# Kernel tuning notes

Hardware: AMD Instinct MI355X
Metric: run time of the kernel (lower is better)

## Reference

```python
import jax, jax.numpy as jnp
import numpy as np

EPS = 1e-5

def conv1x1(x, w, b):
    # x: [B,C,H,W], w: [O,C], b: [O]
    return jnp.einsum('bchw,oc->bohw', x, w) + b[None, :, None, None]

def bn_eval(x, w, b, m, v):
    inv = w / jnp.sqrt(v + EPS)
    return (x - m[None, :, None, None]) * inv[None, :, None, None] + b[None, :, None, None]

def setup_inputs() -> dict:
    key = jax.random.key(0)
    ks = jax.random.split(key, 32)
    B, Fg, Fl, Fi, H, W = 4, 128, 128, 64, 64, 64
    d = {}
    d['g'] = jax.random.normal(ks[0], (B, Fg, H, W), jnp.float32)
    d['x'] = jax.random.normal(ks[1], (B, Fl, H, W), jnp.float32)
    d['wg_w'] = jax.random.normal(ks[2], (Fi, Fg), jnp.float32) * 0.1
    d['wg_b'] = jax.random.normal(ks[3], (Fi,), jnp.float32) * 0.1
    d['bng_w'] = jax.random.uniform(ks[4], (Fi,), jnp.float32)
    d['bng_b'] = jax.random.normal(ks[5], (Fi,), jnp.float32) * 0.1
    d['bng_m'] = jax.random.normal(ks[6], (Fi,), jnp.float32) * 0.1
    d['bng_v'] = jax.random.uniform(ks[7], (Fi,), jnp.float32) + 0.5
    d['wx_w'] = jax.random.normal(ks[8], (Fi, Fl), jnp.float32) * 0.1
    d['wx_b'] = jax.random.normal(ks[9], (Fi,), jnp.float32) * 0.1
    d['bnx_w'] = jax.random.uniform(ks[10], (Fi,), jnp.float32)
    d['bnx_b'] = jax.random.normal(ks[11], (Fi,), jnp.float32) * 0.1
    d['bnx_m'] = jax.random.normal(ks[12], (Fi,), jnp.float32) * 0.1
    d['bnx_v'] = jax.random.uniform(ks[13], (Fi,), jnp.float32) + 0.5
    d['q_w'] = jax.random.normal(ks[14], (Fi // 8, Fi), jnp.float32) * 0.1
    d['q_b'] = jax.random.normal(ks[15], (Fi // 8,), jnp.float32) * 0.1
    d['k_w'] = jax.random.normal(ks[16], (Fi // 8, Fi), jnp.float32) * 0.1
    d['k_b'] = jax.random.normal(ks[17], (Fi // 8,), jnp.float32) * 0.1
    d['v_w'] = jax.random.normal(ks[18], (Fi, Fi), jnp.float32) * 0.1
    d['v_b'] = jax.random.normal(ks[19], (Fi,), jnp.float32) * 0.1
    d['sa_gamma'] = jax.random.normal(ks[20], (1,), jnp.float32)
    d['psi_w'] = jax.random.normal(ks[21], (1, Fi), jnp.float32) * 0.1
    d['psi_b'] = jax.random.normal(ks[22], (1,), jnp.float32) * 0.1
    d['bnp_w'] = jax.random.uniform(ks[23], (1,), jnp.float32)
    d['bnp_b'] = jax.random.normal(ks[24], (1,), jnp.float32) * 0.1
    d['bnp_m'] = jax.random.normal(ks[25], (1,), jnp.float32) * 0.1
    d['bnp_v'] = jax.random.uniform(ks[26], (1,), jnp.float32) + 0.5
    return d

def reference(g, x, wg_w, wg_b, bng_w, bng_b, bng_m, bng_v,
              wx_w, wx_b, bnx_w, bnx_b, bnx_m, bnx_v,
              q_w, q_b, k_w, k_b, v_w, v_b, sa_gamma,
              psi_w, psi_b, bnp_w, bnp_b, bnp_m, bnp_v):
    g1 = bn_eval(conv1x1(g, wg_w, wg_b), bng_w, bng_b, bng_m, bng_v)
    x1 = bn_eval(conv1x1(x, wx_w, wx_b), bnx_w, bnx_b, bnx_m, bnx_v)
    c = jax.nn.relu(g1 + x1)  # [B, Fi, H, W]
    B, C, H, W = c.shape
    N = H * W
    q = conv1x1(c, q_w, q_b).reshape(B, -1, N)  # [B, Fi/8, N]
    k = conv1x1(c, k_w, k_b).reshape(B, -1, N)
    v = conv1x1(c, v_w, v_b).reshape(B, C, N)
    energy = jnp.einsum('bcn,bcm->bnm', q, k)    # [B, N, N]
    attn = jax.nn.softmax(energy, axis=-1)
    sa_out = jnp.einsum('bcm,bnm->bcn', v, attn).reshape(B, C, H, W)
    attended = sa_gamma[0] * sa_out + c
    psi = jax.nn.sigmoid(bn_eval(conv1x1(attended, psi_w, psi_b), bnp_w, bnp_b, bnp_m, bnp_v))
    return x * psi
```

## Files before the change

kernel.cpp:

```cpp
#include <hip/hip_runtime.h>
#include <hip/hip_bf16.h>


typedef short bf16x8 __attribute__((ext_vector_type(8)));
typedef unsigned short u16x8 __attribute__((ext_vector_type(8)));
typedef unsigned short u16x4 __attribute__((ext_vector_type(4)));
typedef float f32x4 __attribute__((ext_vector_type(4)));

__device__ __forceinline__ unsigned short f2b(float f) {
  unsigned u = __builtin_bit_cast(unsigned, f);
  u = (u + 0x7FFFu + ((u >> 16) & 1u)) >> 16;
  return (unsigned short)u;
}

#define EPSV 1e-5f

#define WCAT_OFF   0u
#define WQKV_OFF   32768u
#define BIASC_OFF  44032u
#define BIASQ_OFF  44288u
#define PSIW_OFF   44608u
#define SCAL_OFF   44864u
#define C_OFF      45056u
#define Q_OFF      (C_OFF + 4194304u)
#define K_OFF      (Q_OFF + 262144u)
#define V_OFF      (K_OFF + 262144u)
#define OPART_OFF  (V_OFF + 2097152u)
#define ML_OFF     (OPART_OFF + 16777216u)

__global__ __launch_bounds__(256) void prep_kernel(
    const float* __restrict__ wg_w, const float* __restrict__ wg_b,
    const float* __restrict__ bng_w, const float* __restrict__ bng_b,
    const float* __restrict__ bng_m, const float* __restrict__ bng_v,
    const float* __restrict__ wx_w, const float* __restrict__ wx_b,
    const float* __restrict__ bnx_w, const float* __restrict__ bnx_b,
    const float* __restrict__ bnx_m, const float* __restrict__ bnx_v,
    const float* __restrict__ q_w, const float* __restrict__ q_b,
    const float* __restrict__ k_w, const float* __restrict__ k_b,
    const float* __restrict__ v_w, const float* __restrict__ v_b,
    const float* __restrict__ psi_w, const float* __restrict__ psi_b,
    const float* __restrict__ bnp_w, const float* __restrict__ bnp_b,
    const float* __restrict__ bnp_m, const float* __restrict__ bnp_v,
    const float* __restrict__ sa_gamma,
    unsigned short* __restrict__ Wcat, unsigned short* __restrict__ Wqkv,
    float* __restrict__ bias_c, float* __restrict__ bias_q,
    float* __restrict__ psi_w2, float* __restrict__ scal)
{
  const int t = threadIdx.x;
  const int bid = blockIdx.x;
  if (bid < 16) {
    int o = bid * 4 + (t >> 6);
    int k = (t & 63) * 4;
    float inv;
    const float* src;
    if (k < 128) {
      inv = bng_w[o] * rsqrtf(bng_v[o] + EPSV);
      src = wg_w + o * 128 + k;
    } else {
      inv = bnx_w[o] * rsqrtf(bnx_v[o] + EPSV);
      src = wx_w + o * 128 + (k - 128);
    }
    float4 wv = *(const float4*)src;
    u16x4 pk;
    pk[0] = f2b(wv.x * inv); pk[1] = f2b(wv.y * inv);
    pk[2] = f2b(wv.z * inv); pk[3] = f2b(wv.w * inv);
    *(u16x4*)(Wcat + o * 256 + k) = pk;
    return;
  }
  for (int idx = t; idx < 80 * 64; idx += 256) {
    int r = idx >> 6, k = idx & 63;
    float wv;
    if (r < 8)       wv = q_w[r * 64 + k];
    else if (r < 16) wv = k_w[(r - 8) * 64 + k];
    else             wv = v_w[(r - 16) * 64 + k];
    Wqkv[idx] = f2b(wv);
  }
  if (t < 64) {
    int o = t;
    float invg = bng_w[o] * rsqrtf(bng_v[o] + EPSV);
    float invx = bnx_w[o] * rsqrtf(bnx_v[o] + EPSV);
    bias_c[o] = (wg_b[o] - bng_m[o]) * invg + bng_b[o]
              + (wx_b[o] - bnx_m[o]) * invx + bnx_b[o];
    float invp = bnp_w[0] * rsqrtf(bnp_v[0] + EPSV);
    psi_w2[o] = psi_w[o] * invp;
  }
  if (t < 80)
    bias_q[t] = (t < 8) ? q_b[t] : (t < 16 ? k_b[t - 8] : v_b[t - 16]);
  if (t == 0) {
    float invp = bnp_w[0] * rsqrtf(bnp_v[0] + EPSV);
    scal[0] = sa_gamma[0];
    scal[1] = (psi_b[0] - bnp_m[0]) * invp + bnp_b[0];
  }
}

__global__ __launch_bounds__(256) void conv_qkv_kernel(
    const float* __restrict__ g, const float* __restrict__ x,
    const unsigned short* __restrict__ Wcat, const unsigned short* __restrict__ Wqkv,
    const float* __restrict__ bias_c, const float* __restrict__ bias_q,
    float* __restrict__ c_out, unsigned short* __restrict__ Qb,
    unsigned short* __restrict__ Kb, unsigned short* __restrict__ Vb)
{
  __shared__ __attribute__((aligned(16))) unsigned short xt[32][264];
  __shared__ __attribute__((aligned(16))) unsigned short clds[32][72];

  const int t = threadIdx.x;
  const int bid = blockIdx.x;
  const int b = bid >> 7;
  const int n0 = (bid & 127) << 5;

  {
    const int col4 = t & 7;
    const int rowg = t >> 3;
    float4 v[8];
    #pragma unroll
    for (int rr = 0; rr < 8; ++rr) {
      int row = rowg * 8 + rr;
      const float* src = (row < 128)
          ? (g + ((size_t)(b * 128 + row)) * 4096 + n0 + col4 * 4)
          : (x + ((size_t)(b * 128 + (row - 128))) * 4096 + n0 + col4 * 4);
      v[rr] = *(const float4*)src;
    }
    #pragma unroll
    for (int j = 0; j < 4; ++j) {
      u16x8 pk;
      #pragma unroll
      for (int rr = 0; rr < 8; ++rr)
        pk[rr] = f2b(((const float*)&v[rr])[j]);
      *(u16x8*)(&xt[col4 * 4 + j][rowg * 8]) = pk;
    }
  }
  __syncthreads();

  const int l = t & 63, w = t >> 6;
  const int l15 = l & 15, lg = l >> 4;
  f32x4 zf = {0.f, 0.f, 0.f, 0.f};

  f32x4 acc[2];
  acc[0] = acc[1] = zf;
  const int orow = w * 16 + l15;
  #pragma unroll
  for (int ks = 0; ks < 8; ++ks) {
    bf16x8 af = *(const bf16x8*)(Wcat + orow * 256 + ks * 32 + lg * 8);
    #pragma unroll
    for (int ns = 0; ns < 2; ++ns) {
      bf16x8 bfv = *(const bf16x8*)(&xt[ns * 16 + l15][ks * 32 + lg * 8]);
      acc[ns] = __builtin_amdgcn_mfma_f32_16x16x32_bf16(af, bfv, acc[ns], 0, 0, 0);
    }
  }
  #pragma unroll
  for (int r = 0; r < 4; ++r) {
    int o = w * 16 + lg * 4 + r;
    float bc = bias_c[o];
    #pragma unroll
    for (int ns = 0; ns < 2; ++ns) {
      float cv = fmaxf(acc[ns][r] + bc, 0.f);
      int n = ns * 16 + l15;
      c_out[((size_t)(b * 64 + o)) * 4096 + n0 + n] = cv;
      clds[n][o] = f2b(cv);
    }
  }
  __syncthreads();

  #pragma unroll
  for (int i = 0; i < 3; ++i) {
    int tau = w + 4 * i;
    if (tau >= 10) break;
    int t5 = tau % 5, ns = tau / 5;
    f32x4 a2 = zf;
    #pragma unroll
    for (int kk = 0; kk < 2; ++kk) {
      bf16x8 af = *(const bf16x8*)(Wqkv + (t5 * 16 + l15) * 64 + kk * 32 + lg * 8);
      bf16x8 bfv = *(const bf16x8*)(&clds[ns * 16 + l15][kk * 32 + lg * 8]);
      a2 = __builtin_amdgcn_mfma_f32_16x16x32_bf16(af, bfv, a2, 0, 0, 0);
    }
    #pragma unroll
    for (int r = 0; r < 4; ++r) {
      int row = t5 * 16 + lg * 4 + r;
      int ngl = n0 + ns * 16 + l15;
      float val = a2[r] + bias_q[row];
      if (t5 == 0) {
        if (row < 8) Qb[(((size_t)b << 12) + ngl) * 8 + row] = f2b(val);
        else         Kb[(((size_t)b << 12) + ngl) * 8 + (row - 8)] = f2b(val);
      } else {
        int vch = (t5 - 1) * 16 + lg * 4 + r;
        Vb[((size_t)(b * 64 + vch)) * 4096 + ngl] = f2b(val);
      }
    }
  }
}

__global__ __launch_bounds__(256) void attn_partial_kernel(
    const unsigned short* __restrict__ Qb, const unsigned short* __restrict__ Kb,
    const unsigned short* __restrict__ Vb,
    float* __restrict__ Opart, float* __restrict__ ml)
{
  __shared__ __attribute__((aligned(16))) unsigned short klds[64][8];
  __shared__ __attribute__((aligned(16))) unsigned short vlds[64][72];
  __shared__ __attribute__((aligned(16))) unsigned short plds[4][16][72];

  const int t = threadIdx.x;
  const int bid = blockIdx.x;
  const int qt = bid & 63;
  const int b = (bid >> 6) & 3;
  const int ci = bid >> 8;
  const int n0 = qt << 6;
  const int l = t & 63, w = t >> 6;
  const int l15 = l & 15, lg = l >> 4;

  bf16x8 qf = {0, 0, 0, 0, 0, 0, 0, 0};
  if (lg == 0)
    qf = *(const bf16x8*)(Qb + (((size_t)b << 12) + n0 + w * 16 + l15) * 8);

  f32x4 zf = {0.f, 0.f, 0.f, 0.f};
  f32x4 O[4];
  O[0] = O[1] = O[2] = O[3] = zf;
  float m_run[4] = {-INFINITY, -INFINITY, -INFINITY, -INFINITY};
  float l_run[4] = {0.f, 0.f, 0.f, 0.f};

  const int m_lo = ci << 10, m_hi = (ci + 1) << 10;
  for (int m0 = m_lo; m0 < m_hi; m0 += 64) {
    if (t < 64)
      *(int4*)(&klds[t][0]) = *(const int4*)(Kb + (((size_t)b << 12) + m0 + t) * 8);
    #pragma unroll
    for (int i = 0; i < 2; ++i) {
      int ci2 = t + 256 * i;
      int row = ci2 >> 3, off = ci2 & 7;
      *(int4*)(&vlds[row][off * 8]) =
          *(const int4*)(Vb + ((size_t)(b * 64 + row)) * 4096 + m0 + off * 8);
    }
    __syncthreads();

    f32x4 e[4];
    #pragma unroll
    for (int mt = 0; mt < 4; ++mt) {
      bf16x8 kf = *(const bf16x8*)(&klds[mt * 16 + l15][0]);
      e[mt] = __builtin_amdgcn_mfma_f32_16x16x32_bf16(qf, kf, zf, 0, 0, 0);
    }

    #pragma unroll
    for (int r = 0; r < 4; ++r) {
      float vm = fmaxf(fmaxf(e[0][r], e[1][r]), fmaxf(e[2][r], e[3][r]));
      vm = fmaxf(vm, __shfl_xor(vm, 1));
      vm = fmaxf(vm, __shfl_xor(vm, 2));
      vm = fmaxf(vm, __shfl_xor(vm, 4));
      vm = fmaxf(vm, __shfl_xor(vm, 8));
      float nm = fmaxf(m_run[r], vm);
      float sc = __expf(m_run[r] - nm);
      float s = 0.f;
      #pragma unroll
      for (int mt = 0; mt < 4; ++mt) {
        float p = __expf(e[mt][r] - nm);
        e[mt][r] = p;
        s += p;
      }
      s += __shfl_xor(s, 1);
      s += __shfl_xor(s, 2);
      s += __shfl_xor(s, 4);
      s += __shfl_xor(s, 8);
      l_run[r] = l_run[r] * sc + s;
      m_run[r] = nm;
      #pragma unroll
      for (int mt = 0; mt < 4; ++mt)
        plds[w][lg * 4 + r][mt * 16 + l15] = f2b(e[mt][r]);
      #pragma unroll
      for (int ct = 0; ct < 4; ++ct) O[ct][r] *= sc;
    }

    #pragma unroll
    for (int ct = 0; ct < 4; ++ct) {
      #pragma unroll
      for (int kk = 0; kk < 2; ++kk) {
        bf16x8 pa = *(const bf16x8*)(&plds[w][l15][kk * 32 + lg * 8]);
        bf16x8 vb = *(const bf16x8*)(&vlds[ct * 16 + l15][kk * 32 + lg * 8]);
        O[ct] = __builtin_amdgcn_mfma_f32_16x16x32_bf16(pa, vb, O[ct], 0, 0, 0);
      }
    }
    __syncthreads();
  }

  const size_t pb = ((size_t)(ci * 4 + b)) << 12;
  #pragma unroll
  for (int ct = 0; ct < 4; ++ct) {
    int ch = ct * 16 + l15;
    #pragma unroll
    for (int r = 0; r < 4; ++r) {
      int qg = n0 + w * 16 + lg * 4 + r;
      Opart[(pb + qg) * 64 + ch] = O[ct][r];
    }
  }
  if (l15 == 0) {
    #pragma unroll
    for (int r = 0; r < 4; ++r) {
      int qg = n0 + w * 16 + lg * 4 + r;
      float2 mv;
      mv.x = m_run[r]; mv.y = l_run[r];
      *(float2*)(ml + (pb + qg) * 2) = mv;
    }
  }
}

__global__ __launch_bounds__(256) void combine_kernel(
    const float* __restrict__ Opart, const float* __restrict__ ml,
    const float* __restrict__ c_in, const float* __restrict__ xin,
    const float* __restrict__ psi_w2, const float* __restrict__ scal,
    float* __restrict__ out)
{
  __shared__ __attribute__((aligned(16))) float c_lds[64][68];
  __shared__ float psi_lds[64];

  const int t = threadIdx.x;
  const int bid = blockIdx.x;
  const int b = bid >> 6;
  const int n0 = (bid & 63) << 6;

  #pragma unroll
  for (int i = 0; i < 4; ++i) {
    int idx = t + 256 * i;
    int ch = idx >> 4, c4 = idx & 15;
    float4 cv = *(const float4*)(c_in + ((size_t)(b * 64 + ch)) * 4096 + n0 + c4 * 4);
    *(float4*)(&c_lds[ch][c4 * 4]) = cv;
  }
  __syncthreads();

  const int q = t >> 2, cg = t & 3;
  const int qg = n0 + q;

  float m[4], li[4];
  float M = -INFINITY;
  #pragma unroll
  for (int ci = 0; ci < 4; ++ci) {
    float2 v = *(const float2*)(ml + ((((size_t)(ci * 4 + b)) << 12) + qg) * 2);
    m[ci] = v.x; li[ci] = v.y;
    M = fmaxf(M, v.x);
  }
  float L = 0.f, wgt[4];
  #pragma unroll
  for (int ci = 0; ci < 4; ++ci) {
    wgt[ci] = __expf(m[ci] - M);
    L += wgt[ci] * li[ci];
  }
  float4 o4[4];
  o4[0] = o4[1] = o4[2] = o4[3] = make_float4(0.f, 0.f, 0.f, 0.f);
  #pragma unroll
  for (int ci = 0; ci < 4; ++ci) {
    const float* base = Opart + ((((size_t)(ci * 4 + b)) << 12) + qg) * 64 + cg * 16;
    float wv = wgt[ci];
    #pragma unroll
    for (int k = 0; k < 4; ++k) {
      float4 p = *(const float4*)(base + k * 4);
      o4[k].x += wv * p.x; o4[k].y += wv * p.y;
      o4[k].z += wv * p.z; o4[k].w += wv * p.w;
    }
  }
  const float invL = 1.f / L;
  const float gamma = scal[0], psi_c = scal[1];
  float ps = 0.f;
  #pragma unroll
  for (int k = 0; k < 4; ++k) {
    const float* op = (const float*)&o4[k];
    #pragma unroll
    for (int jj = 0; jj < 4; ++jj) {
      int ch = cg * 16 + k * 4 + jj;
      ps += psi_w2[ch] * (gamma * (op[jj] * invL) + c_lds[ch][q]);
    }
  }
  ps += __shfl_xor(ps, 1);
  ps += __shfl_xor(ps, 2);
  if (cg == 0)
    psi_lds[q] = 1.f / (1.f + __expf(-(ps + psi_c)));
  __syncthreads();

  #pragma unroll
  for (int i = 0; i < 8; ++i) {
    int idx = t + 256 * i;
    int f = idx >> 4, c4 = idx & 15;
    size_t off = ((size_t)(b * 128 + f)) * 4096 + n0 + c4 * 4;
    float4 xv = *(const float4*)(xin + off);
    float4 ov;
    ov.x = xv.x * psi_lds[c4 * 4 + 0];
    ov.y = xv.y * psi_lds[c4 * 4 + 1];
    ov.z = xv.z * psi_lds[c4 * 4 + 2];
    ov.w = xv.w * psi_lds[c4 * 4 + 3];
    *(float4*)(out + off) = ov;
  }
}

extern "C" void kernel_launch(void* const* d_in, const int* in_sizes, int n_in,
                              void* d_out, int out_size, void* d_ws, size_t ws_size,
                              hipStream_t stream) {
  (void)in_sizes; (void)n_in; (void)out_size; (void)ws_size;
  const float* g     = (const float*)d_in[0];
  const float* x     = (const float*)d_in[1];
  const float* wg_w  = (const float*)d_in[2];
  const float* wg_b  = (const float*)d_in[3];
  const float* bng_w = (const float*)d_in[4];
  const float* bng_b = (const float*)d_in[5];
  const float* bng_m = (const float*)d_in[6];
  const float* bng_v = (const float*)d_in[7];
  const float* wx_w  = (const float*)d_in[8];
  const float* wx_b  = (const float*)d_in[9];
  const float* bnx_w = (const float*)d_in[10];
  const float* bnx_b = (const float*)d_in[11];
  const float* bnx_m = (const float*)d_in[12];
  const float* bnx_v = (const float*)d_in[13];
  const float* q_w   = (const float*)d_in[14];
  const float* q_b   = (const float*)d_in[15];
  const float* k_w   = (const float*)d_in[16];
  const float* k_b   = (const float*)d_in[17];
  const float* v_w   = (const float*)d_in[18];
  const float* v_b   = (const float*)d_in[19];
  const float* sa_g  = (const float*)d_in[20];
  const float* psi_w = (const float*)d_in[21];
  const float* psi_b = (const float*)d_in[22];
  const float* bnp_w = (const float*)d_in[23];
  const float* bnp_b = (const float*)d_in[24];
  const float* bnp_m = (const float*)d_in[25];
  const float* bnp_v = (const float*)d_in[26];
  float* out = (float*)d_out;

  char* ws = (char*)d_ws;
  unsigned short* Wcat = (unsigned short*)(ws + WCAT_OFF);
  unsigned short* Wqkv = (unsigned short*)(ws + WQKV_OFF);
  float* bias_c = (float*)(ws + BIASC_OFF);
  float* bias_q = (float*)(ws + BIASQ_OFF);
  float* psiw2  = (float*)(ws + PSIW_OFF);
  float* scal   = (float*)(ws + SCAL_OFF);
  float* c_buf  = (float*)(ws + C_OFF);
  unsigned short* Qb = (unsigned short*)(ws + Q_OFF);
  unsigned short* Kb = (unsigned short*)(ws + K_OFF);
  unsigned short* Vb = (unsigned short*)(ws + V_OFF);
  float* Opart = (float*)(ws + OPART_OFF);
  float* mlb   = (float*)(ws + ML_OFF);

  hipLaunchKernelGGL(prep_kernel, dim3(17), dim3(256), 0, stream,
                     wg_w, wg_b, bng_w, bng_b, bng_m, bng_v,
                     wx_w, wx_b, bnx_w, bnx_b, bnx_m, bnx_v,
                     q_w, q_b, k_w, k_b, v_w, v_b,
                     psi_w, psi_b, bnp_w, bnp_b, bnp_m, bnp_v, sa_g,
                     Wcat, Wqkv, bias_c, bias_q, psiw2, scal);

  hipLaunchKernelGGL(conv_qkv_kernel, dim3(512), dim3(256), 0, stream,
                     g, x, Wcat, Wqkv, bias_c, bias_q, c_buf, Qb, Kb, Vb);

  hipLaunchKernelGGL(attn_partial_kernel, dim3(1024), dim3(256), 0, stream,
                     Qb, Kb, Vb, Opart, mlb);

  hipLaunchKernelGGL(combine_kernel, dim3(256), dim3(256), 0, stream,
                     Opart, mlb, c_buf, x, psiw2, scal, out);
}
```

Before: 188.9 us.

## Store c and partial outputs in bf16, halve tiles, double attention KV splits

Intermediate c and the attention partial outputs are now stored as bf16 rather than fp32, which cuts workspace traffic between kernels. The conv tile shrinks from 32 to 16 pixels and the combine tile from 64 to 16 queries, so those kernels launch more blocks. The attention KV range is split into 8 chunks instead of 4, doubling the grid, and V is staged through LDS for coalesced writes. Rounding c and the partials to bf16 adds precision loss, and combine now reads twice as many partial results.

```diff
diff --git a/kernel.cpp b/kernel.cpp
--- a/kernel.cpp
+++ b/kernel.cpp
@@ -11,6 +11,12 @@
   unsigned u = __builtin_bit_cast(unsigned, f);
   u = (u + 0x7FFFu + ((u >> 16) & 1u)) >> 16;
   return (unsigned short)u;
+}
+__device__ __forceinline__ unsigned short f2b16(float f) {
+  return __builtin_bit_cast(unsigned short, __float2bfloat16(f));
+}
+__device__ __forceinline__ float b2f(unsigned short u) {
+  return __bfloat162float(__builtin_bit_cast(__hip_bfloat16, u));
 }
 
 #define EPSV 1e-5f
@@ -22,7 +28,7 @@
 #define PSIW_OFF   44608u
 #define SCAL_OFF   44864u
 #define C_OFF      45056u
-#define Q_OFF      (C_OFF + 4194304u)
+#define Q_OFF      (C_OFF + 2097152u)
 #define K_OFF      (Q_OFF + 262144u)
 #define V_OFF      (K_OFF + 262144u)
 #define OPART_OFF  (V_OFF + 2097152u)
@@ -97,24 +103,25 @@
     const float* __restrict__ g, const float* __restrict__ x,
     const unsigned short* __restrict__ Wcat, const unsigned short* __restrict__ Wqkv,
     const float* __restrict__ bias_c, const float* __restrict__ bias_q,
-    float* __restrict__ c_out, unsigned short* __restrict__ Qb,
+    unsigned short* __restrict__ cb, unsigned short* __restrict__ Qb,
     unsigned short* __restrict__ Kb, unsigned short* __restrict__ Vb)
 {
-  __shared__ __attribute__((aligned(16))) unsigned short xt[32][264];
-  __shared__ __attribute__((aligned(16))) unsigned short clds[32][72];
+  __shared__ __attribute__((aligned(16))) unsigned short xt[16][264];
+  __shared__ __attribute__((aligned(16))) unsigned short clds[16][72];
+  __shared__ __attribute__((aligned(16))) unsigned short vstage[64][20];
 
   const int t = threadIdx.x;
   const int bid = blockIdx.x;
-  const int b = bid >> 7;
-  const int n0 = (bid & 127) << 5;
+  const int b = bid >> 8;
+  const int n0 = (bid & 255) << 4;
 
   {
-    const int col4 = t & 7;
-    const int rowg = t >> 3;
-    float4 v[8];
-    #pragma unroll
-    for (int rr = 0; rr < 8; ++rr) {
-      int row = rowg * 8 + rr;
+    const int col4 = t & 3;
+    const int rowg = t >> 2;
+    float4 v[4];
+    #pragma unroll
+    for (int rr = 0; rr < 4; ++rr) {
+      int row = rowg * 4 + rr;
       const float* src = (row < 128)
           ? (g + ((size_t)(b * 128 + row)) * 4096 + n0 + col4 * 4)
           : (x + ((size_t)(b * 128 + (row - 128))) * 4096 + n0 + col4 * 4);
@@ -122,11 +129,11 @@
     }
     #pragma unroll
     for (int j = 0; j < 4; ++j) {
-      u16x8 pk;
-      #pragma unroll
-      for (int rr = 0; rr < 8; ++rr)
-        pk[rr] = f2b(((const float*)&v[rr])[j]);
-      *(u16x8*)(&xt[col4 * 4 + j][rowg * 8]) = pk;
+      u16x4 pk;
+      #pragma unroll
+      for (int rr = 0; rr < 4; ++rr)
+        pk[rr] = f2b16(((const float*)&v[rr])[j]);
+      *(u16x4*)(&xt[col4 * 4 + j][rowg * 4]) = pk;
     }
   }
   __syncthreads();
@@ -135,64 +142,67 @@
   const int l15 = l & 15, lg = l >> 4;
   f32x4 zf = {0.f, 0.f, 0.f, 0.f};
 
-  f32x4 acc[2];
-  acc[0] = acc[1] = zf;
+  f32x4 acc = zf;
   const int orow = w * 16 + l15;
   #pragma unroll
   for (int ks = 0; ks < 8; ++ks) {
     bf16x8 af = *(const bf16x8*)(Wcat + orow * 256 + ks * 32 + lg * 8);
-    #pragma unroll
-    for (int ns = 0; ns < 2; ++ns) {
-      bf16x8 bfv = *(const bf16x8*)(&xt[ns * 16 + l15][ks * 32 + lg * 8]);
-      acc[ns] = __builtin_amdgcn_mfma_f32_16x16x32_bf16(af, bfv, acc[ns], 0, 0, 0);
-    }
+    bf16x8 bfv = *(const bf16x8*)(&xt[l15][ks * 32 + lg * 8]);
+    acc = __builtin_amdgcn_mfma_f32_16x16x32_bf16(af, bfv, acc, 0, 0, 0);
   }
   #pragma unroll
   for (int r = 0; r < 4; ++r) {
     int o = w * 16 + lg * 4 + r;
-    float bc = bias_c[o];
-    #pragma unroll
-    for (int ns = 0; ns < 2; ++ns) {
-      float cv = fmaxf(acc[ns][r] + bc, 0.f);
-      int n = ns * 16 + l15;
-      c_out[((size_t)(b * 64 + o)) * 4096 + n0 + n] = cv;
-      clds[n][o] = f2b(cv);
-    }
+    float cv = fmaxf(acc[r] + bias_c[o], 0.f);
+    unsigned short cv16 = f2b16(cv);
+    cb[((size_t)(b * 64 + o)) * 4096 + n0 + l15] = cv16;
+    clds[l15][o] = cv16;
   }
   __syncthreads();
 
-  #pragma unroll
-  for (int i = 0; i < 3; ++i) {
-    int tau = w + 4 * i;
-    if (tau >= 10) break;
-    int t5 = tau % 5, ns = tau / 5;
+  const int ngl = n0 + l15;
+  #pragma unroll
+  for (int i = 0; i < 2; ++i) {
+    int t5 = w + 4 * i;
+    if (t5 >= 5) break;
     f32x4 a2 = zf;
     #pragma unroll
     for (int kk = 0; kk < 2; ++kk) {
       bf16x8 af = *(const bf16x8*)(Wqkv + (t5 * 16 + l15) * 64 + kk * 32 + lg * 8);
-      bf16x8 bfv = *(const bf16x8*)(&clds[ns * 16 + l15][kk * 32 + lg * 8]);
+      bf16x8 bfv = *(const bf16x8*)(&clds[l15][kk * 32 + lg * 8]);
       a2 = __builtin_amdgcn_mfma_f32_16x16x32_bf16(af, bfv, a2, 0, 0, 0);
     }
-    #pragma unroll
-    for (int r = 0; r < 4; ++r) {
-      int row = t5 * 16 + lg * 4 + r;
-      int ngl = n0 + ns * 16 + l15;
-      float val = a2[r] + bias_q[row];
-      if (t5 == 0) {
-        if (row < 8) Qb[(((size_t)b << 12) + ngl) * 8 + row] = f2b(val);
-        else         Kb[(((size_t)b << 12) + ngl) * 8 + (row - 8)] = f2b(val);
-      } else {
-        int vch = (t5 - 1) * 16 + lg * 4 + r;
-        Vb[((size_t)(b * 64 + vch)) * 4096 + ngl] = f2b(val);
+    if (t5 == 0) {
+      u16x4 pk;
+      #pragma unroll
+      for (int r = 0; r < 4; ++r)
+        pk[r] = f2b16(a2[r] + bias_q[lg * 4 + r]);
+      if (lg < 2)
+        *(u16x4*)(Qb + (((size_t)b << 12) + ngl) * 8 + lg * 4) = pk;
+      else
+        *(u16x4*)(Kb + (((size_t)b << 12) + ngl) * 8 + (lg - 2) * 4) = pk;
+    } else {
+      #pragma unroll
+      for (int r = 0; r < 4; ++r) {
+        int row = t5 * 16 + lg * 4 + r;
+        int vch = row - 16;
+        vstage[vch][l15] = f2b16(a2[r] + bias_q[row]);
       }
     }
+  }
+  __syncthreads();
+
+  {
+    int row = t >> 2, seg = t & 3;
+    u16x4 pv = *(const u16x4*)(&vstage[row][seg * 4]);
+    *(u16x4*)(Vb + ((size_t)(b * 64 + row)) * 4096 + n0 + seg * 4) = pv;
   }
 }
 
 __global__ __launch_bounds__(256) void attn_partial_kernel(
     const unsigned short* __restrict__ Qb, const unsigned short* __restrict__ Kb,
     const unsigned short* __restrict__ Vb,
-    float* __restrict__ Opart, float* __restrict__ ml)
+    unsigned short* __restrict__ Opart, float* __restrict__ ml)
 {
   __shared__ __attribute__((aligned(16))) unsigned short klds[64][8];
   __shared__ __attribute__((aligned(16))) unsigned short vlds[64][72];
@@ -217,7 +227,7 @@
   float m_run[4] = {-INFINITY, -INFINITY, -INFINITY, -INFINITY};
   float l_run[4] = {0.f, 0.f, 0.f, 0.f};
 
-  const int m_lo = ci << 10, m_hi = (ci + 1) << 10;
+  const int m_lo = ci << 9, m_hi = (ci + 1) << 9;
   for (int m0 = m_lo; m0 < m_hi; m0 += 64) {
     if (t < 64)
       *(int4*)(&klds[t][0]) = *(const int4*)(Kb + (((size_t)b << 12) + m0 + t) * 8);
@@ -261,7 +271,7 @@
       m_run[r] = nm;
       #pragma unroll
       for (int mt = 0; mt < 4; ++mt)
-        plds[w][lg * 4 + r][mt * 16 + l15] = f2b(e[mt][r]);
+        plds[w][lg * 4 + r][mt * 16 + l15] = f2b16(e[mt][r]);
       #pragma unroll
       for (int ct = 0; ct < 4; ++ct) O[ct][r] *= sc;
     }
@@ -285,7 +295,7 @@
     #pragma unroll
     for (int r = 0; r < 4; ++r) {
       int qg = n0 + w * 16 + lg * 4 + r;
-      Opart[(pb + qg) * 64 + ch] = O[ct][r];
+      Opart[(pb + qg) * 64 + ch] = f2b16(O[ct][r]);
     }
   }
   if (l15 == 0) {
@@ -300,80 +310,71 @@
 }
 
 __global__ __launch_bounds__(256) void combine_kernel(
-    const float* __restrict__ Opart, const float* __restrict__ ml,
-    const float* __restrict__ c_in, const float* __restrict__ xin,
+    const unsigned short* __restrict__ Opart, const float* __restrict__ ml,
+    const unsigned short* __restrict__ cb, const float* __restrict__ xin,
     const float* __restrict__ psi_w2, const float* __restrict__ scal,
     float* __restrict__ out)
 {
-  __shared__ __attribute__((aligned(16))) float c_lds[64][68];
-  __shared__ float psi_lds[64];
+  __shared__ __attribute__((aligned(16))) unsigned short c_lds[64][20];
+  __shared__ __attribute__((aligned(8))) float2 ml_lds[16][8];
+  __shared__ float psi_lds[16];
 
   const int t = threadIdx.x;
   const int bid = blockIdx.x;
-  const int b = bid >> 6;
-  const int n0 = (bid & 63) << 6;
-
-  #pragma unroll
-  for (int i = 0; i < 4; ++i) {
-    int idx = t + 256 * i;
-    int ch = idx >> 4, c4 = idx & 15;
-    float4 cv = *(const float4*)(c_in + ((size_t)(b * 64 + ch)) * 4096 + n0 + c4 * 4);
-    *(float4*)(&c_lds[ch][c4 * 4]) = cv;
+  const int b = bid >> 8;
+  const int n0 = (bid & 255) << 4;
+
+  {
+    int row = t >> 2, seg = t & 3;
+    *(u16x4*)(&c_lds[row][seg * 4]) =
+        *(const u16x4*)(cb + ((size_t)(b * 64 + row)) * 4096 + n0 + seg * 4);
+  }
+  if (t < 128) {
+    int q = t >> 3, ci = t & 7;
+    ml_lds[q][ci] = *(const float2*)(ml + ((((size_t)(ci * 4 + b)) << 12) + n0 + q) * 2);
   }
   __syncthreads();
 
-  const int q = t >> 2, cg = t & 3;
+  const int q = t >> 4, cg = t & 15;
   const int qg = n0 + q;
 
-  float m[4], li[4];
   float M = -INFINITY;
   #pragma unroll
-  for (int ci = 0; ci < 4; ++ci) {
-    float2 v = *(const float2*)(ml + ((((size_t)(ci * 4 + b)) << 12) + qg) * 2);
-    m[ci] = v.x; li[ci] = v.y;
-    M = fmaxf(M, v.x);
-  }
-  float L = 0.f, wgt[4];
-  #pragma unroll
-  for (int ci = 0; ci < 4; ++ci) {
-    wgt[ci] = __expf(m[ci] - M);
-    L += wgt[ci] * li[ci];
-  }
-  float4 o4[4];
-  o4[0] = o4[1] = o4[2] = o4[3] = make_float4(0.f, 0.f, 0.f, 0.f);
-  #pragma unroll
-  for (int ci = 0; ci < 4; ++ci) {
-    const float* base = Opart + ((((size_t)(ci * 4 + b)) << 12) + qg) * 64 + cg * 16;
+  for (int ci = 0; ci < 8; ++ci) M = fmaxf(M, ml_lds[q][ci].x);
+  float L = 0.f, wgt[8];
+  #pragma unroll
+  for (int ci = 0; ci < 8; ++ci) {
+    wgt[ci] = __expf(ml_lds[q][ci].x - M);
+    L += wgt[ci] * ml_lds[q][ci].y;
+  }
+  float o4[4] = {0.f, 0.f, 0.f, 0.f};
+  #pragma unroll
+  for (int ci = 0; ci < 8; ++ci) {
+    u16x4 p = *(const u16x4*)(Opart + ((((size_t)(ci * 4 + b)) << 12) + qg) * 64 + cg * 4);
     float wv = wgt[ci];
     #pragma unroll
-    for (int k = 0; k < 4; ++k) {
-      float4 p = *(const float4*)(base + k * 4);
-      o4[k].x += wv * p.x; o4[k].y += wv * p.y;
-      o4[k].z += wv * p.z; o4[k].w += wv * p.w;
-    }
+    for (int k = 0; k < 4; ++k) o4[k] += wv * b2f(p[k]);
   }
   const float invL = 1.f / L;
   const float gamma = scal[0], psi_c = scal[1];
   float ps = 0.f;
   #pragma unroll
   for (int k = 0; k < 4; ++k) {
-    const float* op = (const float*)&o4[k];
-    #pragma unroll
-    for (int jj = 0; jj < 4; ++jj) {
-      int ch = cg * 16 + k * 4 + jj;
-      ps += psi_w2[ch] * (gamma * (op[jj] * invL) + c_lds[ch][q]);
-    }
+    int ch = cg * 4 + k;
+    ps += psi_w2[ch] * (gamma * (o4[k] * invL) + b2f(c_lds[ch][q]));
   }
   ps += __shfl_xor(ps, 1);
   ps += __shfl_xor(ps, 2);
+  ps += __shfl_xor(ps, 4);
+  ps += __shfl_xor(ps, 8);
   if (cg == 0)
     psi_lds[q] = 1.f / (1.f + __expf(-(ps + psi_c)));
   __syncthreads();
 
   #pragma unroll
-  for (int i = 0; i < 8; ++i) {
+  for (int i = 0; i < 2; ++i) {
     int idx = t + 256 * i;
-    int f = idx >> 4, c4 = idx & 15;
+    int f = idx >> 2, c4 = idx & 3;
     size_t off = ((size_t)(b * 128 + f)) * 4096 + n0 + c4 * 4;
     float4 xv = *(const float4*)(xin + off);
     float4 ov;
@@ -425,11 +426,11 @@
   float* bias_q = (float*)(ws + BIASQ_OFF);
   float* psiw2  = (float*)(ws + PSIW_OFF);
   float* scal   = (float*)(ws + SCAL_OFF);
-  float* c_buf  = (float*)(ws + C_OFF);
+  unsigned short* cb = (unsigned short*)(ws + C_OFF);
   unsigned short* Qb = (unsigned short*)(ws + Q_OFF);
   unsigned short* Kb = (unsigned short*)(ws + K_OFF);
   unsigned short* Vb = (unsigned short*)(ws + V_OFF);
-  float* Opart = (float*)(ws + OPART_OFF);
+  unsigned short* Opart = (unsigned short*)(ws + OPART_OFF);
   float* mlb   = (float*)(ws + ML_OFF);
 
   hipLaunchKernelGGL(prep_kernel, dim3(17), dim3(256), 0, stream,
@@ -439,12 +440,12 @@
                      psi_w, psi_b, bnp_w, bnp_b, bnp_m, bnp_v, sa_g,
                      Wcat, Wqkv, bias_c, bias_q, psiw2, scal);
 
-  hipLaunchKernelGGL(conv_qkv_kernel, dim3(512), dim3(256), 0, stream,
-                     g, x, Wcat, Wqkv, bias_c, bias_q, c_buf, Qb, Kb, Vb);
-
-  hipLaunchKernelGGL(attn_partial_kernel, dim3(1024), dim3(256), 0, stream,
+  hipLaunchKernelGGL(conv_qkv_kernel, dim3(1024), dim3(256), 0, stream,
+                     g, x, Wcat, Wqkv, bias_c, bias_q, cb, Qb, Kb, Vb);
+
+  hipLaunchKernelGGL(attn_partial_kernel, dim3(2048), dim3(256), 0, stream,
                      Qb, Kb, Vb, Opart, mlb);
 
-  hipLaunchKernelGGL(combine_kernel, dim3(256), dim3(256), 0, stream,
-                     Opart, mlb, c_buf, x, psiw2, scal, out);
-}
+  hipLaunchKernelGGL(combine_kernel, dim3(1024), dim3(256), 0, stream,
+                     Opart, mlb, cb, x, psiw2, scal, out);
+}
```

After: 185.6 us. Within noise of the previous version (-1.7%).
